# Kernel tuning notes

Hardware: AMD Instinct MI355X
Metric: run time of the kernel (lower is better)

## Reference

```python
import jax, jax.numpy as jnp
import numpy as np

T, N, F = 8, 384, 32
N_TYPE, MAX_NODE, IN_DIM, HID = 3, 130, 256, 64  # IN_DIM = T*F
C = IN_DIM // 2  # graph channels = conv channels = 128 = MAX_NODE - 2


def setup_inputs():
    key = jax.random.key(0)
    ks = jax.random.split(key, 10)
    V = jax.random.normal(ks[0], (1, T, N, F + 1), dtype=jnp.float32)
    types = (jnp.arange(N) % N_TYPE + 1).astype(jnp.float32)  # exactly 128 nodes per type
    V = V.at[..., -1].set(types)
    graph = jax.random.normal(ks[1], (C, N, N), dtype=jnp.float32)
    u = lambda k, s: jax.random.uniform(k, s, jnp.float32, -0.1, 0.1)
    return dict(
        V=V,
        graph=graph,
        node_type=(jnp.arange(N) % N_TYPE + 1).astype(jnp.int32),
        ex=1,
        lin0_w=u(ks[2], (MAX_NODE // 2, MAX_NODE)),
        lin0_b=u(ks[3], (MAX_NODE // 2,)),
        att_lin_w=u(ks[4], (N_TYPE, HID, IN_DIM)),
        att_lin_b=u(ks[5], (N_TYPE, HID)),
        agg=jax.random.uniform(ks[6], (N_TYPE, 2 * HID, 1), jnp.float32, -1.0, 1.0),
        pl=u(ks[7], (1,)),
        conv2_w=u(ks[8], (C, C, 2, 2)),
        conv2_b=u(ks[9], (C,)),
    )


def _forward(V, graph, lin0_w, lin0_b, att_lin_w, att_lin_b, agg, pl, conv2_w, conv2_b):
    Vs = V[0]                                   # [T, N, F+1]
    t_vec = Vs[0, :, -1].astype(jnp.int32)      # [N], node types in 1..n_type
    feats = jnp.transpose(Vs[:, :, :-1], (1, 0, 2)).reshape(N, T * F)  # [N, T*F]

    # per-type stable gather + zero-pad to MAX_NODE, then node-dim Linear(max_node -> max_node//2)
    def per_type(k):
        mask = t_vec == (k + 1)
        idx = jnp.argsort(jnp.logical_not(mask), stable=True)[:MAX_NODE]
        vk = feats[idx] * mask[idx][:, None].astype(feats.dtype)   # [MAX_NODE, D]
        vk = (vk.T @ lin0_w.T + lin0_b).T                          # [MAX_NODE//2, D]
        return vk

    v = jax.vmap(per_type)(jnp.arange(N_TYPE))  # [n_type, M2, D]

    # TypeAttentionLayer per type idx: linear -> concat with row idx -> agg matmul -> lrelu -> max over nodes -> softmax over types
    def att_layer(Wk, bk, aggk, k):
        x = jnp.einsum('tnd,hd->tnh', v, Wk) + bk               # [n_type, M2, H]
        xi = jnp.take(x, k, axis=0)                             # [M2, H]
        x2 = jnp.concatenate([x, jnp.broadcast_to(xi, x.shape)], axis=-1)  # [n_type, M2, 2H]
        s = jax.nn.leaky_relu(jnp.einsum('tnh,h->tn', x2, aggk[:, 0]))     # slope 0.01, as torch
        return jax.nn.softmax(jnp.max(s, axis=1), axis=0)       # [n_type]

    A = jax.vmap(att_layer)(att_lin_w, att_lin_b, agg, jnp.arange(N_TYPE))  # [n_type, n_type]

    # scatter per-type-pair scores into adjacency: att_mx[i,j] = A[t_i-1, t_j-1]
    att_mx = A[t_vec[:, None] - 1, t_vec[None, :] - 1]          # [N, N]
    wei = graph * att_mx                                        # ablation == 0

    # nb_cnn: zero-pad bottom/right by MAX_NODE - len(graph) = MAX_NODE - C, then valid 2x2 convs back to NxN
    pad = MAX_NODE - C
    wg = jnp.pad(wei, ((0, 0), (0, pad), (0, pad)))
    for _ in range(pad):
        wg = jax.lax.conv_general_dilated(
            wg[None], conv2_w, (1, 1), 'VALID',
            dimension_numbers=('NCHW', 'OIHW', 'NCHW'))[0] + conv2_b[:, None, None]

    out = pl * wg + graph                                       # univ == 2
    return jax.nn.relu(out)                                     # sparse


def reference(V, graph, node_type, ex, lin0_w, lin0_b, att_lin_w, att_lin_b, agg, pl, conv2_w, conv2_b):
    if not ex:
        return None
    return _forward(V, graph, lin0_w, lin0_b, att_lin_w, att_lin_b, agg, pl, conv2_w, conv2_b)
```

## Files before the change

### kernel.cpp

```cpp
#include <hip/hip_runtime.h>

typedef __attribute__((ext_vector_type(8))) short bf16x8;
typedef __attribute__((ext_vector_type(4))) float f32x4;
typedef unsigned int u32;
typedef unsigned short u16;
typedef unsigned long long u64;

#define S0 384
#define PLANE0 (384 * 384)

__device__ __forceinline__ u16 bfr(float f) {
    u32 b = __float_as_uint(f);
    b += 0x7fff + ((b >> 16) & 1);
    return (u16)(b >> 16);
}

__global__ void k_v(const float* __restrict__ V,
                    const float* __restrict__ lin0_w,
                    const float* __restrict__ lin0_b,
                    float* __restrict__ v_out) {
    int blk = blockIdx.x;
    int k = blk / 65, m = blk % 65;
    int d = threadIdx.x;
    int t = d >> 5, f = d & 31;
    const float* vbase = V + (size_t)t * 384 * 33 + f;
    float acc = lin0_b[m];
    for (int r = 0; r < 128; ++r) {
        float w = lin0_w[m * 130 + r];
        acc += w * vbase[(3 * r + k) * 33];
    }
    v_out[(size_t)blk * 256 + d] = acc;
}

__global__ void k_att(const float* __restrict__ v,
                      const float* __restrict__ att_w,
                      const float* __restrict__ att_b,
                      const float* __restrict__ agg,
                      float* __restrict__ A_out) {
    int k = blockIdx.x;
    int tid = threadIdx.x;
    __shared__ float wv1[256], wv2[256];
    __shared__ float sbuf[3][65];
    __shared__ float Ck_s;
    __shared__ float sm[3];
    {
        int d = tid;
        float a1 = 0.f, a2 = 0.f;
        for (int h = 0; h < 64; ++h) {
            float w = att_w[((size_t)(k * 64 + h)) * 256 + d];
            a1 += agg[k * 128 + h] * w;
            a2 += agg[k * 128 + 64 + h] * w;
        }
        wv1[d] = a1;
        wv2[d] = a2;
    }
    if (tid == 0) {
        float c = 0.f;
        for (int h = 0; h < 64; ++h)
            c += (agg[k * 128 + h] + agg[k * 128 + 64 + h]) * att_b[k * 64 + h];
        Ck_s = c;
    }
    __syncthreads();
    if (tid < 195) {
        int t = tid / 65, m = tid % 65;
        const float* vt = v + ((size_t)(t * 65 + m)) * 256;
        const float* vk = v + ((size_t)(k * 65 + m)) * 256;
        float s = Ck_s;
        for (int d = 0; d < 256; ++d)
            s += vt[d] * wv1[d] + vk[d] * wv2[d];
        s = s > 0.f ? s : 0.01f * s;
        sbuf[t][m] = s;
    }
    __syncthreads();
    if (tid < 3) {
        float mx = sbuf[tid][0];
        for (int m = 1; m < 65; ++m) mx = fmaxf(mx, sbuf[tid][m]);
        sm[tid] = mx;
    }
    __syncthreads();
    if (tid == 0) {
        float mx = fmaxf(sm[0], fmaxf(sm[1], sm[2]));
        float e0 = __expf(sm[0] - mx), e1 = __expf(sm[1] - mx), e2 = __expf(sm[2] - mx);
        float inv = 1.f / (e0 + e1 + e2);
        A_out[k * 3 + 0] = e0 * inv;
        A_out[k * 3 + 1] = e1 * inv;
        A_out[k * 3 + 2] = e2 * inv;
    }
}

__global__ void k_prep_E(const float* __restrict__ cw, const float* __restrict__ cb,
                         u16* __restrict__ Ebf, float* __restrict__ beff) {
    int o = blockIdx.x, i = threadIdx.x;
    __shared__ float4 Wo[128];
    __shared__ float red[128];
    Wo[i] = *(const float4*)(cw + (size_t)(o * 128 + i) * 4);
    __syncthreads();
    float a9[9];
#pragma unroll
    for (int q = 0; q < 9; ++q) a9[q] = 0.f;
    for (int m = 0; m < 128; ++m) {
        float4 w1 = *(const float4*)(cw + (size_t)(m * 128 + i) * 4);
        float4 w2 = Wo[m];
        a9[0] += w2.x * w1.x;
        a9[1] += w2.x * w1.y + w2.y * w1.x;
        a9[2] += w2.y * w1.y;
        a9[3] += w2.x * w1.z + w2.z * w1.x;
        a9[4] += w2.x * w1.w + w2.y * w1.z + w2.z * w1.y + w2.w * w1.x;
        a9[5] += w2.y * w1.w + w2.w * w1.y;
        a9[6] += w2.z * w1.z;
        a9[7] += w2.z * w1.w + w2.w * w1.z;
        a9[8] += w2.w * w1.w;
    }
#pragma unroll
    for (int q = 0; q < 9; ++q)
        Ebf[(size_t)o * 1152 + q * 128 + i] = bfr(a9[q]);
    float4 wo = Wo[i];
    red[i] = cb[i] * (wo.x + wo.y + wo.z + wo.w);
    __syncthreads();
    for (int s = 64; s > 0; s >>= 1) {
        if (i < s) red[i] += red[i + s];
        __syncthreads();
    }
    if (i == 0) beff[o] = cb[o] + red[0];
}

__global__ __launch_bounds__(256) void k_conv9(
        const float* __restrict__ graph,
        const short* __restrict__ Ebf,
        const float* __restrict__ A9g,
        const float* __restrict__ beff,
        const float* __restrict__ pl,
        float* __restrict__ out) {
    __shared__ __align__(16) char BtB[4 * 66 * 128];
    const int tid = threadIdx.x;
    const int lane = tid & 63, wave = tid >> 6;
    const int l15 = lane & 15, l16 = lane >> 4;
    const int sp = tid & 15;
    const int hh = (tid >> 4) & 7;
    const int rr = tid >> 7;
    const int y0 = blockIdx.y * 2, x0 = blockIdx.x * 64;
    const int ocbase = wave * 32;

    float fct[4][5];
    int cx[5], rowoff[4];
    {
        int xm[5]; bool cv[5];
#pragma unroll
        for (int j = 0; j < 5; ++j) {
            int x = x0 + sp + 16 * j;
            cv[j] = x < S0;
            cx[j] = cv[j] ? x : S0 - 1;
            xm[j] = x % 3;
        }
#pragma unroll
        for (int r = 0; r < 4; ++r) {
            int y = y0 + r;
            bool rv = y < S0;
            rowoff[r] = (rv ? y : S0 - 1) * S0;
            float a0 = rv ? A9g[(y % 3) * 3 + 0] : 0.f;
            float a1 = rv ? A9g[(y % 3) * 3 + 1] : 0.f;
            float a2 = rv ? A9g[(y % 3) * 3 + 2] : 0.f;
#pragma unroll
            for (int j = 0; j < 5; ++j) {
                float a = (xm[j] == 0) ? a0 : ((xm[j] == 1) ? a1 : a2);
                fct[r][j] = cv[j] ? a : 0.f;
            }
        }
    }

    f32x4 acc[2][2][4];
#pragma unroll
    for (int t2 = 0; t2 < 2; ++t2)
#pragma unroll
        for (int a = 0; a < 2; ++a)
#pragma unroll
            for (int b = 0; b < 4; ++b)
                acc[t2][a][b] = (f32x4){0.f, 0.f, 0.f, 0.f};

#pragma unroll
    for (int ph = 0; ph < 2; ++ph) {
        if (ph) __syncthreads();

        const float* gb = graph + (size_t)(ph * 64 + hh * 8) * PLANE0;
#pragma unroll
        for (int rl = 0; rl < 2; ++rl) {
            int r = rr * 2 + rl;
            const float* gr = gb + rowoff[r];
#pragma unroll
            for (int j = 0; j < 5; ++j) {
                if (j < 4 || sp < 2) {
                    int p = sp + 16 * j;
                    float f = fct[r][j];
                    const float* g0 = gr + cx[j];
                    u16 q[8];
#pragma unroll
                    for (int e = 0; e < 8; ++e)
                        q[e] = bfr(g0[(size_t)e * PLANE0] * f);
                    uint4 w;
                    w.x = (u32)q[0] | ((u32)q[1] << 16);
                    w.y = (u32)q[2] | ((u32)q[3] << 16);
                    w.z = (u32)q[4] | ((u32)q[5] << 16);
                    w.w = (u32)q[6] | ((u32)q[7] << 16);
                    *(uint4*)(BtB + ((r * 66 + p) << 7) + ((hh ^ (p & 7)) << 4)) = w;
                }
            }
        }
        __syncthreads();

#pragma unroll
        for (int tap = 0; tap < 9; ++tap) {
            const int dy = tap / 3, dx = tap % 3;
            const int pm = l15 + dx;
#pragma unroll
            for (int icg = 0; icg < 2; ++icg) {
                const short* Ap = Ebf + (size_t)(ocbase + l15) * 1152
                                  + tap * 128 + ph * 64 + icg * 32 + l16 * 8;
                bf16x8 a0 = *(const bf16x8*)Ap;
                bf16x8 a1 = *(const bf16x8*)(Ap + 16 * 1152);
                const int hs = ((icg * 4 + l16) ^ (pm & 7)) << 4;
#pragma unroll
                for (int t2 = 0; t2 < 2; ++t2) {
#pragma unroll
                    for (int ni = 0; ni < 4; ++ni) {
                        bf16x8 bv = *(const bf16x8*)(BtB
                            + (((t2 + dy) * 66 + ni * 16 + pm) << 7) + hs);
                        acc[t2][0][ni] = __builtin_amdgcn_mfma_f32_16x16x32_bf16(a0, bv, acc[t2][0][ni], 0, 0, 0);
                        acc[t2][1][ni] = __builtin_amdgcn_mfma_f32_16x16x32_bf16(a1, bv, acc[t2][1][ni], 0, 0, 0);
                    }
                }
            }
        }
    }

    float plv = pl[0];
#pragma unroll
    for (int t2 = 0; t2 < 2; ++t2) {
        int yy = y0 + t2;
#pragma unroll
        for (int mi = 0; mi < 2; ++mi) {
#pragma unroll
            for (int r4 = 0; r4 < 4; ++r4) {
                int oc = ocbase + mi * 16 + l16 * 4 + r4;
                float bias = beff[oc];
                const float* grow = graph + (size_t)oc * PLANE0 + (size_t)yy * S0 + x0;
                float* orow = out + (size_t)oc * PLANE0 + (size_t)yy * S0 + x0;
#pragma unroll
                for (int ni = 0; ni < 4; ++ni) {
                    int xx = ni * 16 + l15;
                    float v = plv * (acc[t2][mi][ni][r4] + bias) + grow[xx];
                    orow[xx] = v > 0.f ? v : 0.f;
                }
            }
        }
    }
}

extern "C" void kernel_launch(void* const* d_in, const int* in_sizes, int n_in,
                              void* d_out, int out_size, void* d_ws, size_t ws_size,
                              hipStream_t stream) {
    (void)in_sizes; (void)n_in; (void)out_size; (void)ws_size;
    const float* V      = (const float*)d_in[0];
    const float* graph  = (const float*)d_in[1];
    const float* lin0_w = (const float*)d_in[4];
    const float* lin0_b = (const float*)d_in[5];
    const float* att_w  = (const float*)d_in[6];
    const float* att_b  = (const float*)d_in[7];
    const float* agg    = (const float*)d_in[8];
    const float* pl     = (const float*)d_in[9];
    const float* cw     = (const float*)d_in[10];
    const float* cb     = (const float*)d_in[11];
    float* out = (float*)d_out;

    char* ws = (char*)d_ws;
    float* v_ws = (float*)ws;
    float* A_ws = (float*)(ws + 200704);
    u16*   Ebf  = (u16*)(ws + 200768);
    float* beff = (float*)(ws + 495680);

    k_prep_E<<<128, 128, 0, stream>>>(cw, cb, Ebf, beff);
    k_v<<<195, 256, 0, stream>>>(V, lin0_w, lin0_b, v_ws);
    k_att<<<3, 256, 0, stream>>>(v_ws, att_w, att_b, agg, A_ws);
    k_conv9<<<dim3(6, 192), 256, 0, stream>>>(
        graph, (const short*)Ebf, A_ws, beff, pl, out);
}
```

Baseline: 168.7 us.

## Halve conv tile width, prefetch second channel half, remap blocks across XCDs

```diff
diff --git a/kernel.cpp b/kernel.cpp
--- a/kernel.cpp
+++ b/kernel.cpp
@@ -131,106 +131,174 @@
         const float* __restrict__ beff,
         const float* __restrict__ pl,
         float* __restrict__ out) {
-    __shared__ __align__(16) char BtB[4 * 66 * 128];
+    __shared__ __align__(16) char BtB[17408];
     const int tid = threadIdx.x;
     const int lane = tid & 63, wave = tid >> 6;
     const int l15 = lane & 15, l16 = lane >> 4;
-    const int sp = tid & 15;
-    const int hh = (tid >> 4) & 7;
-    const int rr = tid >> 7;
-    const int y0 = blockIdx.y * 2, x0 = blockIdx.x * 64;
+
+    const int phys = blockIdx.x;
+    const int logical = (phys & 7) * 288 + (phys >> 3);
+    const int bx = logical % 12, by = logical / 12;
+    const int x0 = bx * 32, y0 = by * 2;
     const int ocbase = wave * 32;
 
-    float fct[4][5];
-    int cx[5], rowoff[4];
+    const int spx = tid & 31;
+    const int soct = tid >> 5;
+
+    int rowoff[4];
+    float fr[4][3];
+#pragma unroll
+    for (int r = 0; r < 4; ++r) {
+        int y = y0 + r;
+        bool rv = y < S0;
+        rowoff[r] = (rv ? y : S0 - 1) * S0;
+        int ym = y % 3;
+        fr[r][0] = rv ? A9g[ym * 3 + 0] : 0.f;
+        fr[r][1] = rv ? A9g[ym * 3 + 1] : 0.f;
+        fr[r][2] = rv ? A9g[ym * 3 + 2] : 0.f;
+    }
+    float fct[4];
     {
-        int xm[5]; bool cv[5];
-#pragma unroll
-        for (int j = 0; j < 5; ++j) {
-            int x = x0 + sp + 16 * j;
-            cv[j] = x < S0;
-            cx[j] = cv[j] ? x : S0 - 1;
-            xm[j] = x % 3;
-        }
-#pragma unroll
-        for (int r = 0; r < 4; ++r) {
-            int y = y0 + r;
-            bool rv = y < S0;
-            rowoff[r] = (rv ? y : S0 - 1) * S0;
-            float a0 = rv ? A9g[(y % 3) * 3 + 0] : 0.f;
-            float a1 = rv ? A9g[(y % 3) * 3 + 1] : 0.f;
-            float a2 = rv ? A9g[(y % 3) * 3 + 2] : 0.f;
-#pragma unroll
-            for (int j = 0; j < 5; ++j) {
-                float a = (xm[j] == 0) ? a0 : ((xm[j] == 1) ? a1 : a2);
-                fct[r][j] = cv[j] ? a : 0.f;
+        int xm = (x0 + spx) % 3;
+#pragma unroll
+        for (int r = 0; r < 4; ++r) fct[r] = fr[r][xm];
+    }
+    const float* gmain = graph + (size_t)(soct * 8) * PLANE0 + x0 + spx;
+    const int wmain = (spx << 7) + ((soct ^ (spx & 7)) << 4);
+
+    const float* gext = nullptr;
+    float efct = 0.f;
+    int ewaddr = 0;
+    if (tid < 64) {
+        int erow = tid >> 4;
+        int epx = 32 + ((tid >> 3) & 1);
+        int eoct = tid & 7;
+        int ex = x0 + epx;
+        bool ev = ex < S0;
+        int ecx = ev ? ex : S0 - 1;
+        int exm = ex % 3;
+        efct = ev ? fr[erow][exm] : 0.f;
+        gext = graph + (size_t)(eoct * 8) * PLANE0 + rowoff[erow] + ecx;
+        ewaddr = ((erow * 34 + epx) << 7) + ((eoct ^ (epx & 7)) << 4);
+    }
+
+    f32x4 acc[2][2][2];
+#pragma unroll
+    for (int a = 0; a < 2; ++a)
+#pragma unroll
+        for (int b = 0; b < 2; ++b)
+#pragma unroll
+            for (int c = 0; c < 2; ++c)
+                acc[a][b][c] = (f32x4){0.f, 0.f, 0.f, 0.f};
+
+    float s0[4][8], se0[8];
+#pragma unroll
+    for (int r = 0; r < 4; ++r)
+#pragma unroll
+        for (int e = 0; e < 8; ++e)
+            s0[r][e] = gmain[(size_t)e * PLANE0 + rowoff[r]];
+    if (tid < 64) {
+#pragma unroll
+        for (int e = 0; e < 8; ++e) se0[e] = gext[(size_t)e * PLANE0];
+    }
+
+#pragma unroll
+    for (int r = 0; r < 4; ++r) {
+        uint4 w;
+        w.x = (u32)bfr(s0[r][0] * fct[r]) | ((u32)bfr(s0[r][1] * fct[r]) << 16);
+        w.y = (u32)bfr(s0[r][2] * fct[r]) | ((u32)bfr(s0[r][3] * fct[r]) << 16);
+        w.z = (u32)bfr(s0[r][4] * fct[r]) | ((u32)bfr(s0[r][5] * fct[r]) << 16);
+        w.w = (u32)bfr(s0[r][6] * fct[r]) | ((u32)bfr(s0[r][7] * fct[r]) << 16);
+        *(uint4*)(BtB + ((r * 34) << 7) + wmain) = w;
+    }
+    if (tid < 64) {
+        uint4 w;
+        w.x = (u32)bfr(se0[0] * efct) | ((u32)bfr(se0[1] * efct) << 16);
+        w.y = (u32)bfr(se0[2] * efct) | ((u32)bfr(se0[3] * efct) << 16);
+        w.z = (u32)bfr(se0[4] * efct) | ((u32)bfr(se0[5] * efct) << 16);
+        w.w = (u32)bfr(se0[6] * efct) | ((u32)bfr(se0[7] * efct) << 16);
+        *(uint4*)(BtB + ewaddr) = w;
+    }
+
+    float s1[4][8], se1[8];
+#pragma unroll
+    for (int r = 0; r < 4; ++r)
+#pragma unroll
+        for (int e = 0; e < 8; ++e)
+            s1[r][e] = gmain[(size_t)(64 + e) * PLANE0 + rowoff[r]];
+    if (tid < 64) {
+#pragma unroll
+        for (int e = 0; e < 8; ++e) se1[e] = gext[(size_t)(64 + e) * PLANE0];
+    }
+
+    __syncthreads();
+
+    auto do_mfma = [&](int ph) {
+        const short* Ab = Ebf + (size_t)(ocbase + l15) * 1152 + ph * 64 + l16 * 8;
+        bf16x8 fa[2][2], fn[2][2];
+#pragma unroll
+        for (int icg = 0; icg < 2; ++icg)
+#pragma unroll
+            for (int mi = 0; mi < 2; ++mi)
+                fa[icg][mi] = *(const bf16x8*)(Ab + icg * 32 + mi * (16 * 1152));
+#pragma unroll
+        for (int tap = 0; tap < 9; ++tap) {
+            if (tap < 8) {
+#pragma unroll
+                for (int icg = 0; icg < 2; ++icg)
+#pragma unroll
+                    for (int mi = 0; mi < 2; ++mi)
+                        fn[icg][mi] = *(const bf16x8*)(Ab + (tap + 1) * 128
+                                                       + icg * 32 + mi * (16 * 1152));
             }
-        }
-    }
-
-    f32x4 acc[2][2][4];
-#pragma unroll
-    for (int t2 = 0; t2 < 2; ++t2)
-#pragma unroll
-        for (int a = 0; a < 2; ++a)
-#pragma unroll
-            for (int b = 0; b < 4; ++b)
-                acc[t2][a][b] = (f32x4){0.f, 0.f, 0.f, 0.f};
-
-#pragma unroll
-    for (int ph = 0; ph < 2; ++ph) {
-        if (ph) __syncthreads();
-
-        const float* gb = graph + (size_t)(ph * 64 + hh * 8) * PLANE0;
-#pragma unroll
-        for (int rl = 0; rl < 2; ++rl) {
-            int r = rr * 2 + rl;
-            const float* gr = gb + rowoff[r];
-#pragma unroll
-            for (int j = 0; j < 5; ++j) {
-                if (j < 4 || sp < 2) {
-                    int p = sp + 16 * j;
-                    float f = fct[r][j];
-                    const float* g0 = gr + cx[j];
-                    u16 q[8];
-#pragma unroll
-                    for (int e = 0; e < 8; ++e)
-                        q[e] = bfr(g0[(size_t)e * PLANE0] * f);
-                    uint4 w;
-                    w.x = (u32)q[0] | ((u32)q[1] << 16);
-                    w.y = (u32)q[2] | ((u32)q[3] << 16);
-                    w.z = (u32)q[4] | ((u32)q[5] << 16);
-                    w.w = (u32)q[6] | ((u32)q[7] << 16);
-                    *(uint4*)(BtB + ((r * 66 + p) << 7) + ((hh ^ (p & 7)) << 4)) = w;
-                }
-            }
-        }
-        __syncthreads();
-
-#pragma unroll
-        for (int tap = 0; tap < 9; ++tap) {
             const int dy = tap / 3, dx = tap % 3;
-            const int pm = l15 + dx;
+            const int pbase = l15 + dx;
+            const int pswz = (pbase & 7);
 #pragma unroll
             for (int icg = 0; icg < 2; ++icg) {
-                const short* Ap = Ebf + (size_t)(ocbase + l15) * 1152
-                                  + tap * 128 + ph * 64 + icg * 32 + l16 * 8;
-                bf16x8 a0 = *(const bf16x8*)Ap;
-                bf16x8 a1 = *(const bf16x8*)(Ap + 16 * 1152);
-                const int hs = ((icg * 4 + l16) ^ (pm & 7)) << 4;
+                const int sz = ((icg * 4 + l16) ^ pswz) << 4;
 #pragma unroll
                 for (int t2 = 0; t2 < 2; ++t2) {
 #pragma unroll
-                    for (int ni = 0; ni < 4; ++ni) {
+                    for (int ni = 0; ni < 2; ++ni) {
                         bf16x8 bv = *(const bf16x8*)(BtB
-                            + (((t2 + dy) * 66 + ni * 16 + pm) << 7) + hs);
-                        acc[t2][0][ni] = __builtin_amdgcn_mfma_f32_16x16x32_bf16(a0, bv, acc[t2][0][ni], 0, 0, 0);
-                        acc[t2][1][ni] = __builtin_amdgcn_mfma_f32_16x16x32_bf16(a1, bv, acc[t2][1][ni], 0, 0, 0);
+                            + (((t2 + dy) * 34 + ni * 16 + pbase) << 7) + sz);
+                        acc[t2][0][ni] = __builtin_amdgcn_mfma_f32_16x16x32_bf16(fa[icg][0], bv, acc[t2][0][ni], 0, 0, 0);
+                        acc[t2][1][ni] = __builtin_amdgcn_mfma_f32_16x16x32_bf16(fa[icg][1], bv, acc[t2][1][ni], 0, 0, 0);
                     }
                 }
             }
+#pragma unroll
+            for (int icg = 0; icg < 2; ++icg)
+#pragma unroll
+                for (int mi = 0; mi < 2; ++mi)
+                    fa[icg][mi] = fn[icg][mi];
         }
-    }
+    };
+
+    do_mfma(0);
+    __syncthreads();
+
+#pragma unroll
+    for (int r = 0; r < 4; ++r) {
+        uint4 w;
+        w.x = (u32)bfr(s1[r][0] * fct[r]) | ((u32)bfr(s1[r][1] * fct[r]) << 16);
+        w.y = (u32)bfr(s1[r][2] * fct[r]) | ((u32)bfr(s1[r][3] * fct[r]) << 16);
+        w.z = (u32)bfr(s1[r][4] * fct[r]) | ((u32)bfr(s1[r][5] * fct[r]) << 16);
+        w.w = (u32)bfr(s1[r][6] * fct[r]) | ((u32)bfr(s1[r][7] * fct[r]) << 16);
+        *(uint4*)(BtB + ((r * 34) << 7) + wmain) = w;
+    }
+    if (tid < 64) {
+        uint4 w;
+        w.x = (u32)bfr(se1[0] * efct) | ((u32)bfr(se1[1] * efct) << 16);
+        w.y = (u32)bfr(se1[2] * efct) | ((u32)bfr(se1[3] * efct) << 16);
+        w.z = (u32)bfr(se1[4] * efct) | ((u32)bfr(se1[5] * efct) << 16);
+        w.w = (u32)bfr(se1[6] * efct) | ((u32)bfr(se1[7] * efct) << 16);
+        *(uint4*)(BtB + ewaddr) = w;
+    }
+    __syncthreads();
+
+    do_mfma(1);
 
     float plv = pl[0];
 #pragma unroll
@@ -245,7 +313,7 @@
                 const float* grow = graph + (size_t)oc * PLANE0 + (size_t)yy * S0 + x0;
                 float* orow = out + (size_t)oc * PLANE0 + (size_t)yy * S0 + x0;
 #pragma unroll
-                for (int ni = 0; ni < 4; ++ni) {
+                for (int ni = 0; ni < 2; ++ni) {
                     int xx = ni * 16 + l15;
                     float v = plv * (acc[t2][mi][ni][r4] + bias) + grow[xx];
                     orow[xx] = v > 0.f ? v : 0.f;
@@ -280,6 +348,6 @@
     k_prep_E<<<128, 128, 0, stream>>>(cw, cb, Ebf, beff);
     k_v<<<195, 256, 0, stream>>>(V, lin0_w, lin0_b, v_ws);
     k_att<<<3, 256, 0, stream>>>(v_ws, att_w, att_b, agg, A_ws);
-    k_conv9<<<dim3(6, 192), 256, 0, stream>>>(
+    k_conv9<<<2304, 256, 0, stream>>>(
         graph, (const short*)Ebf, A_ws, beff, pl, out);
 }
```

Result: no change. 169.1 us (+0.2%).

## Pre-pack scaled bf16 graph tiles and stream them into LDS via global_load_lds

Applied to the files above, without the earlier changes.

```diff
diff --git a/kernel.cpp b/kernel.cpp
--- a/kernel.cpp
+++ b/kernel.cpp
@@ -8,6 +8,13 @@
 
 #define S0 384
 #define PLANE0 (384 * 384)
+#define NXT 12
+#define XROWB 10240
+#define XTILEB ((size_t)386 * XROWB)
+
+#define GLOAD_LDS(g, l) __builtin_amdgcn_global_load_lds( \
+    (const __attribute__((address_space(1))) void*)(g),   \
+    (__attribute__((address_space(3))) void*)(l), 16, 0, 0)
 
 __device__ __forceinline__ u16 bfr(float f) {
     u32 b = __float_as_uint(f);
@@ -89,7 +96,7 @@
 }
 
 __global__ void k_prep_E(const float* __restrict__ cw, const float* __restrict__ cb,
-                         u16* __restrict__ Ebf, float* __restrict__ beff) {
+                         u16* __restrict__ Ebf2, float* __restrict__ beff) {
     int o = blockIdx.x, i = threadIdx.x;
     __shared__ float4 Wo[128];
     __shared__ float red[128];
@@ -111,9 +118,10 @@
         a9[7] += w2.z * w1.w + w2.w * w1.z;
         a9[8] += w2.w * w1.w;
     }
+    int icg = i >> 5, el = i & 31;
 #pragma unroll
     for (int q = 0; q < 9; ++q)
-        Ebf[(size_t)o * 1152 + q * 128 + i] = bfr(a9[q]);
+        Ebf2[(size_t)((q * 4 + icg) * 128 + o) * 32 + el] = bfr(a9[q]);
     float4 wo = Wo[i];
     red[i] = cb[i] * (wo.x + wo.y + wo.z + wo.w);
     __syncthreads();
@@ -124,132 +132,124 @@
     if (i == 0) beff[o] = cb[o] + red[0];
 }
 
+__global__ __launch_bounds__(256) void k_pack(
+        const float* __restrict__ graph,
+        const float* __restrict__ A9g,
+        u16* __restrict__ Xbf2) {
+    const int xtile = blockIdx.x, yb = blockIdx.y;
+    const int tid = threadIdx.x;
+    float a9[9];
+#pragma unroll
+    for (int q = 0; q < 9; ++q) a9[q] = A9g[q];
+#pragma unroll
+    for (int i = 0; i < 5; ++i) {
+        int u = tid + i * 256;
+        int r = (u >= 640) ? 1 : 0;
+        int rem = u - r * 640;
+        int p = rem >> 4, j = rem & 15;
+        int y = yb * 2 + r;
+        int x = xtile * 32 + p;
+        int oct = j ^ (p & 15);
+        uint4 w = {0u, 0u, 0u, 0u};
+        if (x < S0 && y < S0) {
+            float f = a9[(y % 3) * 3 + (x % 3)];
+            const float* g0 = graph + (size_t)(oct * 8) * PLANE0 + (size_t)y * S0 + x;
+            u16 q0 = bfr(g0[0 * (size_t)PLANE0] * f);
+            u16 q1 = bfr(g0[1 * (size_t)PLANE0] * f);
+            u16 q2 = bfr(g0[2 * (size_t)PLANE0] * f);
+            u16 q3 = bfr(g0[3 * (size_t)PLANE0] * f);
+            u16 q4 = bfr(g0[4 * (size_t)PLANE0] * f);
+            u16 q5 = bfr(g0[5 * (size_t)PLANE0] * f);
+            u16 q6 = bfr(g0[6 * (size_t)PLANE0] * f);
+            u16 q7 = bfr(g0[7 * (size_t)PLANE0] * f);
+            w.x = (u32)q0 | ((u32)q1 << 16);
+            w.y = (u32)q2 | ((u32)q3 << 16);
+            w.z = (u32)q4 | ((u32)q5 << 16);
+            w.w = (u32)q6 | ((u32)q7 << 16);
+        }
+        *(uint4*)((char*)Xbf2 + (size_t)xtile * XTILEB + (size_t)y * XROWB + rem * 16) = w;
+    }
+}
+
 __global__ __launch_bounds__(256) void k_conv9(
-        const float* __restrict__ graph,
-        const short* __restrict__ Ebf,
-        const float* __restrict__ A9g,
+        const u16* __restrict__ Xbf2,
+        const short* __restrict__ Ebf2,
         const float* __restrict__ beff,
         const float* __restrict__ pl,
+        const float* __restrict__ graph,
         float* __restrict__ out) {
-    __shared__ __align__(16) char BtB[4 * 66 * 128];
+    __shared__ __align__(16) u16 Bt[20480];
     const int tid = threadIdx.x;
     const int lane = tid & 63, wave = tid >> 6;
     const int l15 = lane & 15, l16 = lane >> 4;
-    const int sp = tid & 15;
-    const int hh = (tid >> 4) & 7;
-    const int rr = tid >> 7;
-    const int y0 = blockIdx.y * 2, x0 = blockIdx.x * 64;
-    const int ocbase = wave * 32;
-
-    float fct[4][5];
-    int cx[5], rowoff[4];
+
+    const int phys = blockIdx.x;
+    const int logical = (phys & 7) * 288 + (phys >> 3);
+    const int bx = logical % NXT, by = logical / NXT;
+    const int x0 = bx * 32, y0 = by * 2;
+    const int ocg = wave & 1, rwg = wave >> 1;
+    const int ocbase = ocg * 64;
+
     {
-        int xm[5]; bool cv[5];
-#pragma unroll
-        for (int j = 0; j < 5; ++j) {
-            int x = x0 + sp + 16 * j;
-            cv[j] = x < S0;
-            cx[j] = cv[j] ? x : S0 - 1;
-            xm[j] = x % 3;
-        }
-#pragma unroll
-        for (int r = 0; r < 4; ++r) {
-            int y = y0 + r;
-            bool rv = y < S0;
-            rowoff[r] = (rv ? y : S0 - 1) * S0;
-            float a0 = rv ? A9g[(y % 3) * 3 + 0] : 0.f;
-            float a1 = rv ? A9g[(y % 3) * 3 + 1] : 0.f;
-            float a2 = rv ? A9g[(y % 3) * 3 + 2] : 0.f;
-#pragma unroll
-            for (int j = 0; j < 5; ++j) {
-                float a = (xm[j] == 0) ? a0 : ((xm[j] == 1) ? a1 : a2);
-                fct[r][j] = cv[j] ? a : 0.f;
+        const char* gsrc = (const char*)Xbf2 + (size_t)bx * XTILEB
+                         + (size_t)y0 * XROWB + (size_t)wave * 1024 + lane * 16;
+        char* ldst = (char*)Bt + wave * 1024;
+#pragma unroll
+        for (int i = 0; i < 10; ++i)
+            GLOAD_LDS(gsrc + (size_t)i * 4096, ldst + i * 4096);
+    }
+    __syncthreads();
+
+    f32x4 acc[4][2];
+#pragma unroll
+    for (int a = 0; a < 4; ++a)
+#pragma unroll
+        for (int b = 0; b < 2; ++b)
+            acc[a][b] = (f32x4){0.f, 0.f, 0.f, 0.f};
+
+#pragma unroll
+    for (int tap = 0; tap < 9; ++tap) {
+        const int dy = tap / 3, dx = tap % 3;
+        const int rw = rwg + dy;
+        const int pb = l15 + dx;
+        const int sx = pb & 15;
+#pragma unroll
+        for (int icg = 0; icg < 4; ++icg) {
+            const short* Ap = Ebf2 + ((size_t)((tap * 4 + icg) * 128 + ocbase + l15) << 5)
+                              + l16 * 8;
+            bf16x8 fa0 = *(const bf16x8*)(Ap);
+            bf16x8 fa1 = *(const bf16x8*)(Ap + 512);
+            bf16x8 fa2 = *(const bf16x8*)(Ap + 1024);
+            bf16x8 fa3 = *(const bf16x8*)(Ap + 1536);
+            const int sz = ((icg * 4 + l16) ^ sx) << 4;
+#pragma unroll
+            for (int ni = 0; ni < 2; ++ni) {
+                const bf16x8 bv = *(const bf16x8*)((const char*)Bt
+                    + ((rw * 40 + ni * 16 + pb) << 8) + sz);
+                acc[0][ni] = __builtin_amdgcn_mfma_f32_16x16x32_bf16(fa0, bv, acc[0][ni], 0, 0, 0);
+                acc[1][ni] = __builtin_amdgcn_mfma_f32_16x16x32_bf16(fa1, bv, acc[1][ni], 0, 0, 0);
+                acc[2][ni] = __builtin_amdgcn_mfma_f32_16x16x32_bf16(fa2, bv, acc[2][ni], 0, 0, 0);
+                acc[3][ni] = __builtin_amdgcn_mfma_f32_16x16x32_bf16(fa3, bv, acc[3][ni], 0, 0, 0);
             }
         }
-    }
-
-    f32x4 acc[2][2][4];
-#pragma unroll
-    for (int t2 = 0; t2 < 2; ++t2)
-#pragma unroll
-        for (int a = 0; a < 2; ++a)
-#pragma unroll
-            for (int b = 0; b < 4; ++b)
-                acc[t2][a][b] = (f32x4){0.f, 0.f, 0.f, 0.f};
-
-#pragma unroll
-    for (int ph = 0; ph < 2; ++ph) {
-        if (ph) __syncthreads();
-
-        const float* gb = graph + (size_t)(ph * 64 + hh * 8) * PLANE0;
-#pragma unroll
-        for (int rl = 0; rl < 2; ++rl) {
-            int r = rr * 2 + rl;
-            const float* gr = gb + rowoff[r];
-#pragma unroll
-            for (int j = 0; j < 5; ++j) {
-                if (j < 4 || sp < 2) {
-                    int p = sp + 16 * j;
-                    float f = fct[r][j];
-                    const float* g0 = gr + cx[j];
-                    u16 q[8];
-#pragma unroll
-                    for (int e = 0; e < 8; ++e)
-                        q[e] = bfr(g0[(size_t)e * PLANE0] * f);
-                    uint4 w;
-                    w.x = (u32)q[0] | ((u32)q[1] << 16);
-                    w.y = (u32)q[2] | ((u32)q[3] << 16);
-                    w.z = (u32)q[4] | ((u32)q[5] << 16);
-                    w.w = (u32)q[6] | ((u32)q[7] << 16);
-                    *(uint4*)(BtB + ((r * 66 + p) << 7) + ((hh ^ (p & 7)) << 4)) = w;
-                }
-            }
-        }
-        __syncthreads();
-
-#pragma unroll
-        for (int tap = 0; tap < 9; ++tap) {
-            const int dy = tap / 3, dx = tap % 3;
-            const int pm = l15 + dx;
-#pragma unroll
-            for (int icg = 0; icg < 2; ++icg) {
-                const short* Ap = Ebf + (size_t)(ocbase + l15) * 1152
-                                  + tap * 128 + ph * 64 + icg * 32 + l16 * 8;
-                bf16x8 a0 = *(const bf16x8*)Ap;
-                bf16x8 a1 = *(const bf16x8*)(Ap + 16 * 1152);
-                const int hs = ((icg * 4 + l16) ^ (pm & 7)) << 4;
-#pragma unroll
-                for (int t2 = 0; t2 < 2; ++t2) {
-#pragma unroll
-                    for (int ni = 0; ni < 4; ++ni) {
-                        bf16x8 bv = *(const bf16x8*)(BtB
-                            + (((t2 + dy) * 66 + ni * 16 + pm) << 7) + hs);
-                        acc[t2][0][ni] = __builtin_amdgcn_mfma_f32_16x16x32_bf16(a0, bv, acc[t2][0][ni], 0, 0, 0);
-                        acc[t2][1][ni] = __builtin_amdgcn_mfma_f32_16x16x32_bf16(a1, bv, acc[t2][1][ni], 0, 0, 0);
-                    }
-                }
-            }
-        }
-    }
-
-    float plv = pl[0];
-#pragma unroll
-    for (int t2 = 0; t2 < 2; ++t2) {
-        int yy = y0 + t2;
-#pragma unroll
-        for (int mi = 0; mi < 2; ++mi) {
-#pragma unroll
-            for (int r4 = 0; r4 < 4; ++r4) {
-                int oc = ocbase + mi * 16 + l16 * 4 + r4;
-                float bias = beff[oc];
-                const float* grow = graph + (size_t)oc * PLANE0 + (size_t)yy * S0 + x0;
-                float* orow = out + (size_t)oc * PLANE0 + (size_t)yy * S0 + x0;
-#pragma unroll
-                for (int ni = 0; ni < 4; ++ni) {
-                    int xx = ni * 16 + l15;
-                    float v = plv * (acc[t2][mi][ni][r4] + bias) + grow[xx];
-                    orow[xx] = v > 0.f ? v : 0.f;
-                }
+        __builtin_amdgcn_sched_barrier(0);
+    }
+
+    const float plv = pl[0];
+    const int yy = y0 + rwg;
+#pragma unroll
+    for (int mi = 0; mi < 4; ++mi) {
+#pragma unroll
+        for (int r4 = 0; r4 < 4; ++r4) {
+            const int oc = ocbase + mi * 16 + l16 * 4 + r4;
+            const float bias = beff[oc];
+            const float* grow = graph + (size_t)oc * PLANE0 + (size_t)yy * S0 + x0;
+            float* orow = out + (size_t)oc * PLANE0 + (size_t)yy * S0 + x0;
+#pragma unroll
+            for (int ni = 0; ni < 2; ++ni) {
+                int xx = ni * 16 + l15;
+                float v = plv * (acc[mi][ni][r4] + bias) + grow[xx];
+                orow[xx] = v > 0.f ? v : 0.f;
             }
         }
     }
@@ -272,14 +272,16 @@
     float* out = (float*)d_out;
 
     char* ws = (char*)d_ws;
-    float* v_ws = (float*)ws;
-    float* A_ws = (float*)(ws + 200704);
-    u16*   Ebf  = (u16*)(ws + 200768);
-    float* beff = (float*)(ws + 495680);
-
-    k_prep_E<<<128, 128, 0, stream>>>(cw, cb, Ebf, beff);
+    float* v_ws  = (float*)ws;
+    float* A_ws  = (float*)(ws + 200704);
+    u16*   Ebf2  = (u16*)(ws + 200768);
+    float* beff  = (float*)(ws + 495680);
+    u16*   Xbf2  = (u16*)(ws + 496192);
+
+    k_prep_E<<<128, 128, 0, stream>>>(cw, cb, Ebf2, beff);
     k_v<<<195, 256, 0, stream>>>(V, lin0_w, lin0_b, v_ws);
     k_att<<<3, 256, 0, stream>>>(v_ws, att_w, att_b, agg, A_ws);
-    k_conv9<<<dim3(6, 192), 256, 0, stream>>>(
-        graph, (const short*)Ebf, A_ws, beff, pl, out);
-}
+    k_pack<<<dim3(NXT, 193), 256, 0, stream>>>(graph, A_ws, Xbf2);
+    k_conv9<<<2304, 256, 0, stream>>>(
+        Xbf2, (const short*)Ebf2, beff, pl, graph, out);
+}
```

Result: slower. 204.6 us (+21.3%).
